# Performance work log

Hardware: AMD Instinct MI355X
Metric: run time of the kernel (lower is better)

Reference implementation:

```python
import jax, jax.numpy as jnp
import numpy as np

B, S, N, D = 8, 2048, 512, 1024
MAX_W = 32  # fixed max span width (inclusive widths 0..MAX_W-1)
MASK_FILL = -1000.0


def setup_inputs() -> dict:
    key = jax.random.key(0)
    k1, k2, k3, k4 = jax.random.split(key, 4)
    sequence_tensor = jax.random.normal(k1, (B, S, D), dtype=jnp.float32)
    starts = jax.random.randint(k2, (B, N), 0, S - MAX_W)
    widths = jax.random.randint(k3, (B, N), 0, MAX_W)  # inclusive width = widths
    span_indices = jnp.stack([starts, starts + widths], axis=-1)  # (B, N, 2)
    att_w = jax.random.normal(k4, (D, 1), dtype=jnp.float32) * 0.02
    att_b = jnp.zeros((1,), dtype=jnp.float32)
    return {"sequence_tensor": sequence_tensor, "span_indices": span_indices,
            "att_w": att_w, "att_b": att_b}


def reference(sequence_tensor, span_indices, att_w, att_b):
    dtype = sequence_tensor.dtype
    starts = span_indices[..., 0]               # (B, N)
    ends = span_indices[..., 1]                 # (B, N), inclusive
    widths = ends - starts                      # (B, N)

    rng = jnp.arange(MAX_W)                     # (W,)
    raw_idx = ends[..., None] - rng             # (B, N, W), walks backward from end
    span_mask = (rng <= widths[..., None]) & (raw_idx >= 0)  # (B, N, W)
    idx = jnp.maximum(raw_idx, 0)               # relu on indices

    # global attention logits: (B, S, 1)
    logits = sequence_tensor @ att_w + att_b

    b, n = idx.shape[0], idx.shape[1]
    flat = idx.reshape(b, n * MAX_W)            # (B, N*W)
    # gather embeddings and logits over the time axis
    span_emb = jnp.take_along_axis(sequence_tensor, flat[..., None], axis=1)
    span_emb = span_emb.reshape(b, n, MAX_W, -1)              # (B, N, W, D)
    span_logits = jnp.take_along_axis(logits[..., 0], flat, axis=1)
    span_logits = span_logits.reshape(b, n, MAX_W)            # (B, N, W)

    # memory-efficient masked softmax: fill masked logits with -1000
    masked_logits = jnp.where(span_mask, span_logits, jnp.asarray(MASK_FILL, dtype))
    attn = jax.nn.softmax(masked_logits, axis=-1)             # (B, N, W)

    # weighted-sum pooling over span positions
    return jnp.einsum('bnw,bnwd->bnd', attn, span_emb)
```

## Files before the change

### kernel.cpp

```cpp
#include <hip/hip_runtime.h>
#include <hip/hip_bf16.h>

#define B 8
#define S 2048
#define N 512
#define D 1024
#define MAX_W 32
#define MASK_FILL -1000.0f

typedef float vfloat4 __attribute__((ext_vector_type(4)));

__device__ inline unsigned short f2bf(float f) {
    unsigned u = __float_as_uint(f);
    u += 0x7fff + ((u >> 16) & 1);
    return (unsigned short)(u >> 16);
}

__global__ __launch_bounds__(512) void prep_kernel(
    const float* __restrict__ seq,
    const float* __restrict__ att_w,
    const float* __restrict__ att_b,
    float* __restrict__ logits,
    unsigned short* __restrict__ seqh)
{
    const int row  = blockIdx.x * 8 + (threadIdx.x >> 6);
    const int lane = threadIdx.x & 63;

    const float4* rp = (const float4*)(seq + (size_t)row * D);
    const float4* wp = (const float4*)att_w;

    float4 a[4];
    float acc = 0.0f;
#pragma unroll
    for (int k = 0; k < 4; ++k) {
        a[k] = rp[lane + 64 * k];
        const float4 w = wp[lane + 64 * k];
        acc += a[k].x * w.x + a[k].y * w.y + a[k].z * w.z + a[k].w * w.w;
    }

    ushort4* hp = (ushort4*)(seqh + (size_t)row * D);
#pragma unroll
    for (int k = 0; k < 4; ++k) {
        ushort4 h;
        h.x = f2bf(a[k].x); h.y = f2bf(a[k].y);
        h.z = f2bf(a[k].z); h.w = f2bf(a[k].w);
        hp[lane + 64 * k] = h;
    }

#pragma unroll
    for (int off = 32; off > 0; off >>= 1)
        acc += __shfl_down(acc, off);
    if (lane == 0)
        logits[row] = acc + att_b[0];
}

__global__ __launch_bounds__(256) void pool_kernel(
    const unsigned short* __restrict__ seqh,
    const int*   __restrict__ spans,
    const float* __restrict__ logits,
    float* __restrict__ out)
{
    const int b    = blockIdx.x & 7;
    const int n    = blockIdx.x >> 3;
    const int span = b * N + n;

    const int start = spans[2 * span + 0];
    const int end   = spans[2 * span + 1];
    const int width = end - start;

    __shared__ float s_attn[MAX_W];
    __shared__ int   s_idx[MAX_W];

    const int tid = threadIdx.x;

    if (tid < MAX_W) {
        const int w   = tid;
        const int raw = end - w;
        const bool valid = (w <= width) && (raw >= 0);
        const int idx = raw > 0 ? raw : 0;
        const float l = valid ? logits[b * S + idx] : MASK_FILL;

        float m = l;
#pragma unroll
        for (int off = 16; off > 0; off >>= 1)
            m = fmaxf(m, __shfl_down(m, off, 32));
        m = __shfl(m, 0, 32);

        const float p = __expf(l - m);

        float sum = p;
#pragma unroll
        for (int off = 16; off > 0; off >>= 1)
            sum += __shfl_down(sum, off, 32);
        sum = __shfl(sum, 0, 32);

        s_attn[w] = p / sum;
        s_idx[w]  = idx;
    }
    __syncthreads();

    const unsigned short* sb = seqh + (size_t)b * S * D;

    float4 acc = make_float4(0.f, 0.f, 0.f, 0.f);

    const int cnt  = width + 1;
    const int cnt4 = (cnt + 3) & ~3;

    for (int w = 0; w < cnt4; w += 4) {
        const float a0 = s_attn[w + 0];
        const float a1 = s_attn[w + 1];
        const float a2 = s_attn[w + 2];
        const float a3 = s_attn[w + 3];
        const int   i0 = s_idx[w + 0];
        const int   i1 = s_idx[w + 1];
        const int   i2 = s_idx[w + 2];
        const int   i3 = s_idx[w + 3];

        const uint2 q0 = ((const uint2*)(sb + (size_t)i0 * D))[tid];
        const uint2 q1 = ((const uint2*)(sb + (size_t)i1 * D))[tid];
        const uint2 q2 = ((const uint2*)(sb + (size_t)i2 * D))[tid];
        const uint2 q3 = ((const uint2*)(sb + (size_t)i3 * D))[tid];

#define BL(u) __uint_as_float((u) << 16)
#define BH(u) __uint_as_float((u) & 0xffff0000u)
        acc.x += a0 * BL(q0.x) + a1 * BL(q1.x) + a2 * BL(q2.x) + a3 * BL(q3.x);
        acc.y += a0 * BH(q0.x) + a1 * BH(q1.x) + a2 * BH(q2.x) + a3 * BH(q3.x);
        acc.z += a0 * BL(q0.y) + a1 * BL(q1.y) + a2 * BL(q2.y) + a3 * BL(q3.y);
        acc.w += a0 * BH(q0.y) + a1 * BH(q1.y) + a2 * BH(q2.y) + a3 * BH(q3.y);
#undef BL
#undef BH
    }

    vfloat4 va;
    va.x = acc.x; va.y = acc.y; va.z = acc.z; va.w = acc.w;
    vfloat4* op = ((vfloat4*)(out + (size_t)span * D)) + tid;
    __builtin_nontemporal_store(va, op);
}

extern "C" void kernel_launch(void* const* d_in, const int* in_sizes, int n_in,
                              void* d_out, int out_size, void* d_ws, size_t ws_size,
                              hipStream_t stream)
{
    const float* seq    = (const float*)d_in[0];
    const int*   spans  = (const int*)  d_in[1];
    const float* att_w  = (const float*)d_in[2];
    const float* att_b  = (const float*)d_in[3];

    float* out    = (float*)d_out;
    float* logits = (float*)d_ws;
    unsigned short* seqh =
        (unsigned short*)((char*)d_ws + (size_t)B * S * sizeof(float));

    prep_kernel<<<(B * S) / 8, 512, 0, stream>>>(seq, att_w, att_b,
                                                 logits, seqh);
    pool_kernel<<<B * N, 256, 0, stream>>>(seqh, spans, logits, out);
}
```

Measured before the change: 119.9 us.

## Split span rows across two thread halves with 16-byte loads and LDS reduction

The pool kernel now has each thread load 16 bytes (8 bf16) per row instead of 8. The two halves of the 256-thread block process interleaved span positions, and the partial sums are combined through shared memory before the output store. The aim is wider loads per instruction, twice the rows in flight per iteration, and fewer issued memory instructions. In exchange it adds an LDS round trip and barrier, leaves half the threads idle during the store, and pads the width to a multiple of 8 instead of 4.

Result: no change. 117.9 us (-1.7%).

```diff
diff --git a/kernel.cpp b/kernel.cpp
--- a/kernel.cpp
+++ b/kernel.cpp
@@ -70,8 +70,11 @@
 
     __shared__ float s_attn[MAX_W];
     __shared__ int   s_idx[MAX_W];
+    __shared__ float s_part[128][9];
 
-    const int tid = threadIdx.x;
+    const int tid  = threadIdx.x;
+    const int c    = tid & 127;
+    const int half = tid >> 7;
 
     if (tid < MAX_W) {
         const int w   = tid;
@@ -101,40 +104,59 @@
 
     const unsigned short* sb = seqh + (size_t)b * S * D;
 
-    float4 acc = make_float4(0.f, 0.f, 0.f, 0.f);
+    float acc[8];
+#pragma unroll
+    for (int j = 0; j < 8; ++j) acc[j] = 0.0f;
 
     const int cnt  = width + 1;
-    const int cnt4 = (cnt + 3) & ~3;
+    const int cnt8 = (cnt + 7) & ~7;
 
-    for (int w = 0; w < cnt4; w += 4) {
-        const float a0 = s_attn[w + 0];
-        const float a1 = s_attn[w + 1];
-        const float a2 = s_attn[w + 2];
-        const float a3 = s_attn[w + 3];
-        const int   i0 = s_idx[w + 0];
-        const int   i1 = s_idx[w + 1];
-        const int   i2 = s_idx[w + 2];
-        const int   i3 = s_idx[w + 3];
+    for (int w = 0; w < cnt8; w += 8) {
+        const int w0 = w + half;
+        const float a0 = s_attn[w0 + 0];
+        const float a1 = s_attn[w0 + 2];
+        const float a2 = s_attn[w0 + 4];
+        const float a3 = s_attn[w0 + 6];
+        const int   i0 = s_idx[w0 + 0];
+        const int   i1 = s_idx[w0 + 2];
+        const int   i2 = s_idx[w0 + 4];
+        const int   i3 = s_idx[w0 + 6];
 
-        const uint2 q0 = ((const uint2*)(sb + (size_t)i0 * D))[tid];
-        const uint2 q1 = ((const uint2*)(sb + (size_t)i1 * D))[tid];
-        const uint2 q2 = ((const uint2*)(sb + (size_t)i2 * D))[tid];
-        const uint2 q3 = ((const uint2*)(sb + (size_t)i3 * D))[tid];
+        const uint4 q0 = ((const uint4*)(sb + (size_t)i0 * D))[c];
+        const uint4 q1 = ((const uint4*)(sb + (size_t)i1 * D))[c];
+        const uint4 q2 = ((const uint4*)(sb + (size_t)i2 * D))[c];
+        const uint4 q3 = ((const uint4*)(sb + (size_t)i3 * D))[c];
 
 #define BL(u) __uint_as_float((u) << 16)
 #define BH(u) __uint_as_float((u) & 0xffff0000u)
-        acc.x += a0 * BL(q0.x) + a1 * BL(q1.x) + a2 * BL(q2.x) + a3 * BL(q3.x);
-        acc.y += a0 * BH(q0.x) + a1 * BH(q1.x) + a2 * BH(q2.x) + a3 * BH(q3.x);
-        acc.z += a0 * BL(q0.y) + a1 * BL(q1.y) + a2 * BL(q2.y) + a3 * BL(q3.y);
-        acc.w += a0 * BH(q0.y) + a1 * BH(q1.y) + a2 * BH(q2.y) + a3 * BH(q3.y);
+        acc[0] += a0 * BL(q0.x) + a1 * BL(q1.x) + a2 * BL(q2.x) + a3 * BL(q3.x);
+        acc[1] += a0 * BH(q0.x) + a1 * BH(q1.x) + a2 * BH(q2.x) + a3 * BH(q3.x);
+        acc[2] += a0 * BL(q0.y) + a1 * BL(q1.y) + a2 * BL(q2.y) + a3 * BL(q3.y);
+        acc[3] += a0 * BH(q0.y) + a1 * BH(q1.y) + a2 * BH(q2.y) + a3 * BH(q3.y);
+        acc[4] += a0 * BL(q0.z) + a1 * BL(q1.z) + a2 * BL(q2.z) + a3 * BL(q3.z);
+        acc[5] += a0 * BH(q0.z) + a1 * BH(q1.z) + a2 * BH(q2.z) + a3 * BH(q3.z);
+        acc[6] += a0 * BL(q0.w) + a1 * BL(q1.w) + a2 * BL(q2.w) + a3 * BL(q3.w);
+        acc[7] += a0 * BH(q0.w) + a1 * BH(q1.w) + a2 * BH(q2.w) + a3 * BH(q3.w);
 #undef BL
 #undef BH
     }
 
-    vfloat4 va;
-    va.x = acc.x; va.y = acc.y; va.z = acc.z; va.w = acc.w;
-    vfloat4* op = ((vfloat4*)(out + (size_t)span * D)) + tid;
-    __builtin_nontemporal_store(va, op);
+    if (half == 1) {
+#pragma unroll
+        for (int j = 0; j < 8; ++j) s_part[c][j] = acc[j];
+    }
+    __syncthreads();
+    if (half == 0) {
+#pragma unroll
+        for (int j = 0; j < 8; ++j) acc[j] += s_part[c][j];
+
+        vfloat4 va;
+        va.x = acc[0]; va.y = acc[1]; va.z = acc[2]; va.w = acc[3];
+        vfloat4* op = ((vfloat4*)(out + (size_t)span * D)) + 2 * c;
+        __builtin_nontemporal_store(va, op);
+        va.x = acc[4]; va.y = acc[5]; va.z = acc[6]; va.w = acc[7];
+        __builtin_nontemporal_store(va, op + 1);
+    }
 }
 
 extern "C" void kernel_launch(void* const* d_in, const int* in_sizes, int n_in,
```
